# Performance work log

Measured on AMD Instinct MI355X. Metric: run time of the kernel, lower is better.

## Reference

```python
import jax, jax.numpy as jnp
import numpy as np

B, S, D_IN, D_H = 8, 4096, 256, 512
EPS = 1e-6


def setup_inputs() -> dict:
    key = jax.random.key(0)
    ks = jax.random.split(key, 5)
    scale = 1.0 / np.sqrt(D_IN)  # torch Linear default init scale (uniform bound)
    x = jax.random.normal(ks[0], (B, S, D_IN), dtype=jnp.float32)
    Wi = jax.random.normal(ks[1], (D_IN, D_H), dtype=jnp.float32) * scale
    Wf = jax.random.normal(ks[2], (D_IN, D_H), dtype=jnp.float32) * scale
    Wo = jax.random.normal(ks[3], (D_IN, D_H), dtype=jnp.float32) * scale
    Wz = jax.random.normal(ks[4], (D_IN, D_H), dtype=jnp.float32) * scale
    zb = jnp.zeros((D_H,), dtype=jnp.float32)
    return {"x": x, "Wi": Wi, "bi": zb, "Wf": Wf, "bf": zb,
            "Wo": Wo, "bo": zb, "Wz": Wz, "bz": zb}


def _xlstm_forward(x, Wi, bi, Wf, bf, Wo, bo, Wz, bz):
    # Batched projections over all timesteps at once: [B,S,D_H] each.
    i_t = jnp.exp(jnp.clip(jnp.einsum('bsd,dh->bsh', x, Wi) + bi, -20.0, 0.0))
    f_t = jnp.exp(jnp.clip(jnp.einsum('bsd,dh->bsh', x, Wf) + bf, -20.0, 0.0))
    o_t = jax.nn.sigmoid(jnp.einsum('bsd,dh->bsh', x, Wo) + bo)
    z_t = jnp.tanh(jnp.einsum('bsd,dh->bsh', x, Wz) + bz)

    def step(carry, gates):
        c, n = carry
        i, f, o, z = gates
        c = f * c + i * z
        n = f * n + i
        h = o * (c / (n + EPS))
        return (c, n), h

    c0 = jnp.zeros((x.shape[0], Wi.shape[1]), dtype=x.dtype)
    n0 = jnp.ones((x.shape[0], Wi.shape[1]), dtype=x.dtype)
    # time-major scan over the recurrence
    gates_tm = tuple(jnp.swapaxes(g, 0, 1) for g in (i_t, f_t, o_t, z_t))  # [S,B,H]
    _, h_tm = jax.lax.scan(step, (c0, n0), gates_tm)
    return jnp.swapaxes(h_tm, 0, 1)  # [B,S,H]


def reference(x, Wi, bi, Wf, bf, Wo, bo, Wz, bz):
    return _xlstm_forward(x, Wi, bi, Wf, bf, Wo, bo, Wz, bz)
```

## Files before the change

### kernel.cpp

```cpp
#include <hip/hip_runtime.h>
#include <hip/hip_bf16.h>
#include <cstdint>
#include <cstddef>

typedef __hip_bfloat16 bf16;
typedef __attribute__((ext_vector_type(8))) short short8;
typedef __attribute__((ext_vector_type(4))) short short4v;
typedef __attribute__((ext_vector_type(4))) float floatx4;

#define BB 8
#define SS 4096
#define DIN 256
#define DH 512
#define NCH 256
#define CHUNK 16

__device__ __forceinline__ float sh2f(short v) {
    unsigned int u = ((unsigned int)(unsigned short)v) << 16;
    float f; __builtin_memcpy(&f, &u, 4); return f;
}
__device__ __forceinline__ float frcp(float x) { return __builtin_amdgcn_rcpf(x); }
__device__ __forceinline__ short f2sh(float a) {
    bf16 bv = __float2bfloat16(a);
    short sv; __builtin_memcpy(&sv, &bv, 2); return sv;
}

__global__ __launch_bounds__(256) void convert_x(
    const float* __restrict__ X, bf16* __restrict__ Xb)
{
    const int idx = blockIdx.x * 256 + threadIdx.x;
    float4 v = ((const float4*)X)[idx];
    bf16 o[4] = {__float2bfloat16(v.x), __float2bfloat16(v.y),
                 __float2bfloat16(v.z), __float2bfloat16(v.w)};
    ((short4v*)Xb)[idx] = *(const short4v*)o;
}

__global__ __launch_bounds__(256) void transpose_w(
    const float* __restrict__ Wi, const float* __restrict__ Wf,
    const float* __restrict__ Wo, const float* __restrict__ Wz,
    bf16* __restrict__ Wt)
{
    int o = blockIdx.x * 256 + threadIdx.x;
    int r = o >> 8;
    int k = o & 255;
    int y = r >> 7;
    int c = r & 127;
    int g = c >> 5;
    int h = y * 32 + (c & 31);
    const float* W = (g == 0) ? Wi : (g == 1) ? Wf : (g == 2) ? Wo : Wz;
    Wt[o] = __float2bfloat16(W[(size_t)k * DH + h]);
}

__device__ __forceinline__ void load16_lds(const bf16* g, short* l)
{
    __builtin_amdgcn_global_load_lds(
        (const __attribute__((address_space(1))) unsigned int*)g,
        (__attribute__((address_space(3))) unsigned int*)l,
        16, 0, 0);
}

template<int MODE>
__global__ __launch_bounds__(256) void gemm_fused(
    const bf16* __restrict__ Xb, const bf16* __restrict__ Wt,
    const float* __restrict__ bi, const float* __restrict__ bfv,
    const float* __restrict__ bo, const float* __restrict__ bz,
    float* __restrict__ Aa, float* __restrict__ Bca, float* __restrict__ Bna,
    float* __restrict__ out, int nb)
{
    __shared__ __align__(16) short smem[128 * 132];

    const int cpx = gridDim.x >> 3;
    const int logical = ((int)blockIdx.x & 7) * cpx + ((int)blockIdx.x >> 3);
    const int y  = logical & 15;
    const int m0 = (logical >> 4) * 128;
    const int n0 = y * 128;

    const int tid  = threadIdx.x;
    const int wave = tid >> 6, lane = tid & 63;
    const int wm   = (wave >> 1) * 64, wn = (wave & 1) * 64;
    const int l15  = lane & 15;
    const int q    = lane >> 4;

    floatx4 acc[4][4];
#pragma unroll
    for (int i = 0; i < 4; i++)
#pragma unroll
        for (int j = 0; j < 4; j++) acc[i][j] = (floatx4){0.f, 0.f, 0.f, 0.f};

    const int r_ld = tid >> 2;
    const int c_ld = tid & 3;
    const bf16* agp0 = Xb + (size_t)(m0 + r_ld) * DIN + c_ld * 8;
    const bf16* agp1 = Xb + (size_t)(m0 + 64 + r_ld) * DIN + c_ld * 8;
    const bf16* bgp0 = Wt + (size_t)(n0 + r_ld) * DIN + c_ld * 8;
    const bf16* bgp1 = Wt + (size_t)(n0 + 64 + r_ld) * DIN + c_ld * 8;

#define STAGE(K0, BUF)                                            \
    do {                                                          \
        short* A_ = smem + (BUF) * 8192;                          \
        short* B_ = A_ + 4096;                                    \
        load16_lds(agp0 + (K0), &A_[tid * 8]);                    \
        load16_lds(agp1 + (K0), &A_[2048 + tid * 8]);             \
        load16_lds(bgp0 + (K0), &B_[tid * 8]);                    \
        load16_lds(bgp1 + (K0), &B_[2048 + tid * 8]);             \
    } while (0)

    STAGE(0, 0);
    asm volatile("s_waitcnt vmcnt(0)" ::: "memory");
    __builtin_amdgcn_s_barrier();

#pragma unroll
    for (int k = 0; k < 8; k++) {
        const int cur = k & 1;
        if (k < 7) STAGE((k + 1) * 32, cur ^ 1);
        const short* A = smem + cur * 8192;
        const short* B = A + 4096;
        short8 af[4], bfr[4];
#pragma unroll
        for (int ti = 0; ti < 4; ti++)
            af[ti] = *(const short8*)&A[(wm + ti * 16 + l15) * 32 + q * 8];
#pragma unroll
        for (int tj = 0; tj < 4; tj++)
            bfr[tj] = *(const short8*)&B[(wn + tj * 16 + l15) * 32 + q * 8];
#pragma unroll
        for (int ti = 0; ti < 4; ti++)
#pragma unroll
            for (int tj = 0; tj < 4; tj++)
                acc[ti][tj] = __builtin_amdgcn_mfma_f32_16x16x32_bf16(
                    af[ti], bfr[tj], acc[ti][tj], 0, 0, 0);
        asm volatile("s_waitcnt vmcnt(0) lgkmcnt(0)" ::: "memory");
        __builtin_amdgcn_s_barrier();
    }
#undef STAGE

#pragma unroll
    for (int ti = 0; ti < 4; ti++) {
        const int mrow = wm + ti * 16 + q * 4;
#pragma unroll
        for (int tj = 0; tj < 4; tj++) {
            const int cb = wn + tj * 16;
            const int g  = cb >> 5;
            if (MODE == 0 && g == 2) continue;
            const int c  = cb + l15;
            const float* bp = (g == 0) ? bi : (g == 1) ? bfv
                            : (g == 2) ? bo : bz;
            const float bsv = bp[y * 32 + (c & 31)];
#pragma unroll
            for (int r = 0; r < 4; r++) {
                const float v = acc[ti][tj][r] + bsv;
                float a;
                if (g == 0 || g == 1) {
                    a = __expf(fminf(fmaxf(v, -20.f), 0.f));
                } else if (g == 2) {
                    a = frcp(1.f + __expf(-v));
                } else {
                    a = 1.f - 2.f * frcp(__expf(2.f * v) + 1.f);
                }
                smem[(mrow + r) * 132 + c] = f2sh(a);
            }
        }
    }
    __syncthreads();

    const int bidx = m0 / SS;
    const int hh   = tid & 31;
    const int ch   = tid >> 5;
    const int ch_g = ((m0 % SS) >> 4) + ch;
    const size_t cidx = (size_t)(ch_g * nb + bidx) * DH + y * 32 + hh;
    const short* base = &smem[(ch * CHUNK) * 132];

    if (MODE == 0) {
        float A = 1.f, Bc = 0.f, Bn = 0.f;
#pragma unroll
        for (int s = 0; s < CHUNK; s++) {
            const short* rp = base + s * 132;
            const float iv = sh2f(rp[hh]);
            const float f  = sh2f(rp[32 + hh]);
            const float zv = sh2f(rp[96 + hh]);
            Bc = fmaf(f, Bc, iv * zv);
            Bn = fmaf(f, Bn, iv);
            A *= f;
        }
        Aa[cidx] = A; Bca[cidx] = Bc; Bna[cidx] = Bn;
    } else {
        float c = Aa[cidx];
        float n = Bca[cidx];
        float* orow = out + (size_t)(m0 + ch * CHUNK) * DH + y * 32 + hh;
#pragma unroll
        for (int s = 0; s < CHUNK; s++) {
            const short* rp = base + s * 132;
            const float iv = sh2f(rp[hh]);
            const float f  = sh2f(rp[32 + hh]);
            const float ov = sh2f(rp[64 + hh]);
            const float zv = sh2f(rp[96 + hh]);
            c = fmaf(f, c, iv * zv);
            n = fmaf(f, n, iv);
            orow[(size_t)s * DH] = ov * c * frcp(n + 1e-6f);
        }
    }
}

__global__ __launch_bounds__(256) void scan_chunks(
    float* __restrict__ Aa, float* __restrict__ Bca,
    const float* __restrict__ Bna, int nb)
{
    __shared__ float sA[4][64], sBc[4][64], sBn[4][64];
    const int tid = threadIdx.x;
    const int t   = blockIdx.x * 64 + (tid & 63);
    const int s   = tid >> 6;
    const int stride = nb * DH;
    const int SEG = NCH / 4;

    float A = 1.f, Bc = 0.f, Bn = 0.f;
    for (int k = 0; k < SEG; k++) {
        const size_t cidx = (size_t)(s * SEG + k) * stride + t;
        const float a  = Aa[cidx];
        const float bc = Bca[cidx];
        const float bn = Bna[cidx];
        Bc = fmaf(a, Bc, bc);
        Bn = fmaf(a, Bn, bn);
        A *= a;
    }
    sA[s][tid & 63] = A; sBc[s][tid & 63] = Bc; sBn[s][tid & 63] = Bn;
    __syncthreads();

    float c = 0.f, n = 1.f;
#pragma unroll
    for (int s2 = 0; s2 < 3; s2++) {
        if (s2 < s) {
            const float a  = sA[s2][tid & 63];
            const float nc = fmaf(a, c, sBc[s2][tid & 63]);
            n = fmaf(a, n, sBn[s2][tid & 63]);
            c = nc;
        }
    }

    for (int k = 0; k < SEG; k++) {
        const size_t cidx = (size_t)(s * SEG + k) * stride + t;
        const float a  = Aa[cidx];
        const float bc = Bca[cidx];
        const float bn = Bna[cidx];
        Aa[cidx] = c; Bca[cidx] = n;
        const float nc = fmaf(a, c, bc);
        n = fmaf(a, n, bn);
        c = nc;
    }
}

extern "C" void kernel_launch(void* const* d_in, const int* in_sizes, int n_in,
                              void* d_out, int out_size, void* d_ws, size_t ws_size,
                              hipStream_t stream)
{
    const float* x   = (const float*)d_in[0];
    const float* Wi  = (const float*)d_in[1];
    const float* bi  = (const float*)d_in[2];
    const float* Wf  = (const float*)d_in[3];
    const float* bfv = (const float*)d_in[4];
    const float* Wo  = (const float*)d_in[5];
    const float* bo  = (const float*)d_in[6];
    const float* Wz  = (const float*)d_in[7];
    const float* bz  = (const float*)d_in[8];
    float* out = (float*)d_out;

    int nb = BB;
    while (nb > 1) {
        size_t need = (1u << 20)
                    + (size_t)nb * SS * DIN * 2
                    + 3 * (size_t)NCH * nb * DH * 4;
        if (need <= ws_size) break;
        nb >>= 1;
    }

    bf16* Wt = (bf16*)d_ws;
    bf16* Xb = (bf16*)((char*)d_ws + (1u << 20));
    float* Aa  = (float*)(Xb + (size_t)nb * SS * DIN);
    float* Bca = Aa  + (size_t)NCH * nb * DH;
    float* Bna = Bca + (size_t)NCH * nb * DH;

    transpose_w<<<2048, 256, 0, stream>>>(Wi, Wf, Wo, Wz, Wt);

    for (int b0 = 0; b0 < BB; b0 += nb) {
        const float* Xsrc = x   + (size_t)b0 * SS * DIN;
        float*       Ob   = out + (size_t)b0 * SS * DH;
        convert_x<<<nb * 1024, 256, 0, stream>>>(Xsrc, Xb);
        gemm_fused<0><<<nb * 512, 256, 0, stream>>>(
            Xb, Wt, bi, bfv, bo, bz, Aa, Bca, Bna, nullptr, nb);
        scan_chunks<<<nb * 8, 256, 0, stream>>>(Aa, Bca, Bna, nb);
        gemm_fused<1><<<nb * 512, 256, 0, stream>>>(
            Xb, Wt, bi, bfv, bo, bz, Aa, Bca, Bna, Ob, nb);
    }
}
```

Measured before the change: 241.8 us.

## Fuse two-pass GEMM and chunk scan into single-pass decoupled-lookback kernel

Replaces the two-pass scheme (a GEMM with state computation, a separate scan kernel, then a second GEMM pass) with one GEMM kernel. Blocks take ordered tickets through an atomic counter and pass the carried (c, n) state to the next time tile of the same chain through flags in global memory. This removes the second GEMM over all inputs and the separate scan launch. It also merges the weight transpose, x conversion and flag reset into one prep kernel. The cost is a serial dependency chain of 32 tiles per (batch, column-group) with spin-waits between them, which may expose latency.

After: 488.9 us. +102.2%, slower.

```diff
diff --git a/kernel.cpp b/kernel.cpp
--- a/kernel.cpp
+++ b/kernel.cpp
@@ -12,7 +12,6 @@
 #define SS 4096
 #define DIN 256
 #define DH 512
-#define NCH 256
 #define CHUNK 16
 
 __device__ __forceinline__ float sh2f(short v) {
@@ -25,30 +24,36 @@
     short sv; __builtin_memcpy(&sv, &bv, 2); return sv;
 }
 
-__global__ __launch_bounds__(256) void convert_x(
-    const float* __restrict__ X, bf16* __restrict__ Xb)
-{
-    const int idx = blockIdx.x * 256 + threadIdx.x;
-    float4 v = ((const float4*)X)[idx];
-    bf16 o[4] = {__float2bfloat16(v.x), __float2bfloat16(v.y),
-                 __float2bfloat16(v.z), __float2bfloat16(v.w)};
-    ((short4v*)Xb)[idx] = *(const short4v*)o;
-}
-
-__global__ __launch_bounds__(256) void transpose_w(
+__global__ __launch_bounds__(256) void prep(
     const float* __restrict__ Wi, const float* __restrict__ Wf,
     const float* __restrict__ Wo, const float* __restrict__ Wz,
-    bf16* __restrict__ Wt)
-{
-    int o = blockIdx.x * 256 + threadIdx.x;
-    int r = o >> 8;
-    int k = o & 255;
-    int y = r >> 7;
-    int c = r & 127;
-    int g = c >> 5;
-    int h = y * 32 + (c & 31);
-    const float* W = (g == 0) ? Wi : (g == 1) ? Wf : (g == 2) ? Wo : Wz;
-    Wt[o] = __float2bfloat16(W[(size_t)k * DH + h]);
+    bf16* __restrict__ Wt,
+    const float* __restrict__ X, bf16* __restrict__ Xb,
+    unsigned int* __restrict__ Flag,
+    int tblk, int cblk, int nwords)
+{
+    const int bx = blockIdx.x;
+    const int tid = threadIdx.x;
+    if (bx < tblk) {
+        int o = bx * 256 + tid;
+        int r = o >> 8;
+        int k = o & 255;
+        int y = r >> 7;
+        int c = r & 127;
+        int g = c >> 5;
+        int h = y * 32 + (c & 31);
+        const float* W = (g == 0) ? Wi : (g == 1) ? Wf : (g == 2) ? Wo : Wz;
+        Wt[o] = __float2bfloat16(W[(size_t)k * DH + h]);
+    } else if (bx < tblk + cblk) {
+        const int idx = (bx - tblk) * 256 + tid;
+        float4 v = ((const float4*)X)[idx];
+        bf16 o[4] = {__float2bfloat16(v.x), __float2bfloat16(v.y),
+                     __float2bfloat16(v.z), __float2bfloat16(v.w)};
+        ((short4v*)Xb)[idx] = *(const short4v*)o;
+    } else {
+        const int i = (bx - tblk - cblk) * 256 + tid;
+        if (i < nwords) Flag[i] = 0u;
+    }
 }
 
 __device__ __forceinline__ void load16_lds(const bf16* g, short* l)
@@ -59,23 +64,33 @@
         16, 0, 0);
 }
 
-template<int MODE>
-__global__ __launch_bounds__(256) void gemm_fused(
+__global__ __launch_bounds__(256) void gemm_scan(
     const bf16* __restrict__ Xb, const bf16* __restrict__ Wt,
     const float* __restrict__ bi, const float* __restrict__ bfv,
     const float* __restrict__ bo, const float* __restrict__ bz,
-    float* __restrict__ Aa, float* __restrict__ Bca, float* __restrict__ Bna,
-    float* __restrict__ out, int nb)
+    float* __restrict__ Inc, unsigned int* __restrict__ Flag,
+    unsigned int* __restrict__ Tick,
+    float* __restrict__ out, int chShift)
 {
     __shared__ __align__(16) short smem[128 * 132];
-
-    const int cpx = gridDim.x >> 3;
-    const int logical = ((int)blockIdx.x & 7) * cpx + ((int)blockIdx.x >> 3);
-    const int y  = logical & 15;
-    const int m0 = (logical >> 4) * 128;
-    const int n0 = y * 128;
+    __shared__ float cA[8][32], cBc[8][32], cBn[8][32];
+    __shared__ float sc[8][32], sn[8][32];
+    __shared__ int s_ticket;
 
     const int tid  = threadIdx.x;
+    if (tid == 0)
+        s_ticket = (int)__hip_atomic_fetch_add(Tick, 1u, __ATOMIC_RELAXED,
+                                               __HIP_MEMORY_SCOPE_AGENT);
+    __syncthreads();
+    const int t     = s_ticket;
+    const int CH    = 1 << chShift;
+    const int chain = t & (CH - 1);
+    const int mt    = t >> chShift;
+    const int b     = chain >> 4;
+    const int y     = chain & 15;
+    const int m0    = (b * 32 + mt) * 128;
+    const int n0    = y * 128;
+
     const int wave = tid >> 6, lane = tid & 63;
     const int wm   = (wave >> 1) * 64, wn = (wave & 1) * 64;
     const int l15  = lane & 15;
@@ -139,7 +154,6 @@
         for (int tj = 0; tj < 4; tj++) {
             const int cb = wn + tj * 16;
             const int g  = cb >> 5;
-            if (MODE == 0 && g == 2) continue;
             const int c  = cb + l15;
             const float* bp = (g == 0) ? bi : (g == 1) ? bfv
                             : (g == 2) ? bo : bz;
@@ -161,14 +175,11 @@
     }
     __syncthreads();
 
-    const int bidx = m0 / SS;
-    const int hh   = tid & 31;
-    const int ch   = tid >> 5;
-    const int ch_g = ((m0 % SS) >> 4) + ch;
-    const size_t cidx = (size_t)(ch_g * nb + bidx) * DH + y * 32 + hh;
+    const int hh = tid & 31;
+    const int ch = tid >> 5;
     const short* base = &smem[(ch * CHUNK) * 132];
 
-    if (MODE == 0) {
+    {
         float A = 1.f, Bc = 0.f, Bn = 0.f;
 #pragma unroll
         for (int s = 0; s < CHUNK; s++) {
@@ -180,10 +191,42 @@
             Bn = fmaf(f, Bn, iv);
             A *= f;
         }
-        Aa[cidx] = A; Bca[cidx] = Bc; Bna[cidx] = Bn;
-    } else {
-        float c = Aa[cidx];
-        float n = Bca[cidx];
+        cA[ch][hh] = A; cBc[ch][hh] = Bc; cBn[ch][hh] = Bn;
+    }
+    __syncthreads();
+
+    if (tid < 32) {
+        float c = 0.f, n = 1.f;
+        if (mt > 0) {
+            const int pt = t - CH;
+            while (__hip_atomic_load(Flag + pt, __ATOMIC_ACQUIRE,
+                                     __HIP_MEMORY_SCOPE_AGENT) == 0u)
+                __builtin_amdgcn_s_sleep(2);
+            c = __hip_atomic_load(Inc + (size_t)pt * 64 + hh,
+                                  __ATOMIC_RELAXED, __HIP_MEMORY_SCOPE_AGENT);
+            n = __hip_atomic_load(Inc + (size_t)pt * 64 + 32 + hh,
+                                  __ATOMIC_RELAXED, __HIP_MEMORY_SCOPE_AGENT);
+        }
+#pragma unroll
+        for (int k = 0; k < 8; k++) {
+            sc[k][hh] = c; sn[k][hh] = n;
+            const float a  = cA[k][hh];
+            const float nc = fmaf(a, c, cBc[k][hh]);
+            n = fmaf(a, n, cBn[k][hh]);
+            c = nc;
+        }
+        __hip_atomic_store(Inc + (size_t)t * 64 + hh, c,
+                           __ATOMIC_RELAXED, __HIP_MEMORY_SCOPE_AGENT);
+        __hip_atomic_store(Inc + (size_t)t * 64 + 32 + hh, n,
+                           __ATOMIC_RELAXED, __HIP_MEMORY_SCOPE_AGENT);
+        __hip_atomic_store(Flag + t, 1u,
+                           __ATOMIC_RELEASE, __HIP_MEMORY_SCOPE_AGENT);
+    }
+    __syncthreads();
+
+    {
+        float c = sc[ch][hh];
+        float n = sn[ch][hh];
         float* orow = out + (size_t)(m0 + ch * CHUNK) * DH + y * 32 + hh;
 #pragma unroll
         for (int s = 0; s < CHUNK; s++) {
@@ -196,53 +239,6 @@
             n = fmaf(f, n, iv);
             orow[(size_t)s * DH] = ov * c * frcp(n + 1e-6f);
         }
-    }
-}
-
-__global__ __launch_bounds__(256) void scan_chunks(
-    float* __restrict__ Aa, float* __restrict__ Bca,
-    const float* __restrict__ Bna, int nb)
-{
-    __shared__ float sA[4][64], sBc[4][64], sBn[4][64];
-    const int tid = threadIdx.x;
-    const int t   = blockIdx.x * 64 + (tid & 63);
-    const int s   = tid >> 6;
-    const int stride = nb * DH;
-    const int SEG = NCH / 4;
-
-    float A = 1.f, Bc = 0.f, Bn = 0.f;
-    for (int k = 0; k < SEG; k++) {
-        const size_t cidx = (size_t)(s * SEG + k) * stride + t;
-        const float a  = Aa[cidx];
-        const float bc = Bca[cidx];
-        const float bn = Bna[cidx];
-        Bc = fmaf(a, Bc, bc);
-        Bn = fmaf(a, Bn, bn);
-        A *= a;
-    }
-    sA[s][tid & 63] = A; sBc[s][tid & 63] = Bc; sBn[s][tid & 63] = Bn;
-    __syncthreads();
-
-    float c = 0.f, n = 1.f;
-#pragma unroll
-    for (int s2 = 0; s2 < 3; s2++) {
-        if (s2 < s) {
-            const float a  = sA[s2][tid & 63];
-            const float nc = fmaf(a, c, sBc[s2][tid & 63]);
-            n = fmaf(a, n, sBn[s2][tid & 63]);
-            c = nc;
-        }
-    }
-
-    for (int k = 0; k < SEG; k++) {
-        const size_t cidx = (size_t)(s * SEG + k) * stride + t;
-        const float a  = Aa[cidx];
-        const float bc = Bca[cidx];
-        const float bn = Bna[cidx];
-        Aa[cidx] = c; Bca[cidx] = n;
-        const float nc = fmaf(a, c, bc);
-        n = fmaf(a, n, bn);
-        c = nc;
     }
 }
 
@@ -265,27 +261,31 @@
     while (nb > 1) {
         size_t need = (1u << 20)
                     + (size_t)nb * SS * DIN * 2
-                    + 3 * (size_t)NCH * nb * DH * 4;
+                    + (size_t)nb * 512 * 64 * 4
+                    + ((size_t)nb * 512 + 1) * 4;
         if (need <= ws_size) break;
         nb >>= 1;
     }
 
     bf16* Wt = (bf16*)d_ws;
     bf16* Xb = (bf16*)((char*)d_ws + (1u << 20));
-    float* Aa  = (float*)(Xb + (size_t)nb * SS * DIN);
-    float* Bca = Aa  + (size_t)NCH * nb * DH;
-    float* Bna = Bca + (size_t)NCH * nb * DH;
-
-    transpose_w<<<2048, 256, 0, stream>>>(Wi, Wf, Wo, Wz, Wt);
+    float* Inc = (float*)(Xb + (size_t)nb * SS * DIN);
+    unsigned int* Flag = (unsigned int*)(Inc + (size_t)nb * 512 * 64);
+    unsigned int* Tick = Flag + (size_t)nb * 512;
+
+    int chShift = 4;
+    { int v = nb * 16; chShift = 31 - __builtin_clz(v); }
 
     for (int b0 = 0; b0 < BB; b0 += nb) {
         const float* Xsrc = x   + (size_t)b0 * SS * DIN;
         float*       Ob   = out + (size_t)b0 * SS * DH;
-        convert_x<<<nb * 1024, 256, 0, stream>>>(Xsrc, Xb);
-        gemm_fused<0><<<nb * 512, 256, 0, stream>>>(
-            Xb, Wt, bi, bfv, bo, bz, Aa, Bca, Bna, nullptr, nb);
-        scan_chunks<<<nb * 8, 256, 0, stream>>>(Aa, Bca, Bna, nb);
-        gemm_fused<1><<<nb * 512, 256, 0, stream>>>(
-            Xb, Wt, bi, bfv, bo, bz, Aa, Bca, Bna, Ob, nb);
-    }
-}
+        const int tblk   = (b0 == 0) ? 2048 : 0;
+        const int cblk   = nb * 1024;
+        const int nwords = nb * 512 + 1;
+        const int fblk   = (nwords + 255) / 256;
+        prep<<<tblk + cblk + fblk, 256, 0, stream>>>(
+            Wi, Wf, Wo, Wz, Wt, Xsrc, Xb, Flag, tblk, cblk, nwords);
+        gemm_scan<<<nb * 512, 256, 0, stream>>>(
+            Xb, Wt, bi, bfv, bo, bz, Inc, Flag, Tick, Ob, chShift);
+    }
+}
```

## Fuse transpose, convert, two GEMM passes and scan into one cooperative kernel

Applied to the files above, without the earlier changes.

Replaces the five separate launches (weight transpose, x conversion, GEMM pass 0, chunk scan, GEMM pass 1) with a single persistent cooperative kernel that separates the phases with grid-wide syncs. GEMM tiles are walked in a grid-stride loop sized to occupancy. The aim is to remove launch gaps and tail effects between the stages. In exchange it adds grid-sync cost, fixes the grid size by occupancy, and runs the scan phase on only a few blocks while the rest sit idle.

After: 512.5 us. +111.9%, slower.

```diff
diff --git a/kernel.cpp b/kernel.cpp
--- a/kernel.cpp
+++ b/kernel.cpp
@@ -1,7 +1,10 @@
 #include <hip/hip_runtime.h>
+#include <hip/hip_cooperative_groups.h>
 #include <hip/hip_bf16.h>
 #include <cstdint>
 #include <cstddef>
+
+namespace cg = cooperative_groups;
 
 typedef __hip_bfloat16 bf16;
 typedef __attribute__((ext_vector_type(8))) short short8;
@@ -25,32 +28,6 @@
     short sv; __builtin_memcpy(&sv, &bv, 2); return sv;
 }
 
-__global__ __launch_bounds__(256) void convert_x(
-    const float* __restrict__ X, bf16* __restrict__ Xb)
-{
-    const int idx = blockIdx.x * 256 + threadIdx.x;
-    float4 v = ((const float4*)X)[idx];
-    bf16 o[4] = {__float2bfloat16(v.x), __float2bfloat16(v.y),
-                 __float2bfloat16(v.z), __float2bfloat16(v.w)};
-    ((short4v*)Xb)[idx] = *(const short4v*)o;
-}
-
-__global__ __launch_bounds__(256) void transpose_w(
-    const float* __restrict__ Wi, const float* __restrict__ Wf,
-    const float* __restrict__ Wo, const float* __restrict__ Wz,
-    bf16* __restrict__ Wt)
-{
-    int o = blockIdx.x * 256 + threadIdx.x;
-    int r = o >> 8;
-    int k = o & 255;
-    int y = r >> 7;
-    int c = r & 127;
-    int g = c >> 5;
-    int h = y * 32 + (c & 31);
-    const float* W = (g == 0) ? Wi : (g == 1) ? Wf : (g == 2) ? Wo : Wz;
-    Wt[o] = __float2bfloat16(W[(size_t)k * DH + h]);
-}
-
 __device__ __forceinline__ void load16_lds(const bf16* g, short* l)
 {
     __builtin_amdgcn_global_load_lds(
@@ -60,19 +37,17 @@
 }
 
 template<int MODE>
-__global__ __launch_bounds__(256) void gemm_fused(
+__device__ __forceinline__ void gemm_tile(
+    short* __restrict__ smem, int logical, int nb,
     const bf16* __restrict__ Xb, const bf16* __restrict__ Wt,
     const float* __restrict__ bi, const float* __restrict__ bfv,
     const float* __restrict__ bo, const float* __restrict__ bz,
     float* __restrict__ Aa, float* __restrict__ Bca, float* __restrict__ Bna,
-    float* __restrict__ out, int nb)
+    float* __restrict__ out)
 {
-    __shared__ __align__(16) short smem[128 * 132];
-
-    const int cpx = gridDim.x >> 3;
-    const int logical = ((int)blockIdx.x & 7) * cpx + ((int)blockIdx.x >> 3);
     const int y  = logical & 15;
-    const int m0 = (logical >> 4) * 128;
+    const int gm = logical >> 4;
+    const int m0 = gm * 128;
     const int n0 = y * 128;
 
     const int tid  = threadIdx.x;
@@ -93,6 +68,8 @@
     const bf16* agp1 = Xb + (size_t)(m0 + 64 + r_ld) * DIN + c_ld * 8;
     const bf16* bgp0 = Wt + (size_t)(n0 + r_ld) * DIN + c_ld * 8;
     const bf16* bgp1 = Wt + (size_t)(n0 + 64 + r_ld) * DIN + c_ld * 8;
+
+    __syncthreads();
 
 #define STAGE(K0, BUF)                                            \
     do {                                                          \
@@ -199,50 +176,107 @@
     }
 }
 
-__global__ __launch_bounds__(256) void scan_chunks(
-    float* __restrict__ Aa, float* __restrict__ Bca,
-    const float* __restrict__ Bna, int nb)
+extern "C" __global__ void __launch_bounds__(256) fused_all(
+    const float* __restrict__ Wi, const float* __restrict__ Wf,
+    const float* __restrict__ Wo, const float* __restrict__ Wz,
+    const float* __restrict__ X,
+    bf16* __restrict__ Wt, bf16* __restrict__ Xb,
+    const float* __restrict__ bi, const float* __restrict__ bfv,
+    const float* __restrict__ bo, const float* __restrict__ bz,
+    float* __restrict__ Aa, float* __restrict__ Bca, float* __restrict__ Bna,
+    float* __restrict__ out, int nb, int doTrans)
 {
-    __shared__ float sA[4][64], sBc[4][64], sBn[4][64];
+    __shared__ __align__(16) short smem[128 * 132];
+    cg::grid_group grid = cg::this_grid();
+
     const int tid = threadIdx.x;
-    const int t   = blockIdx.x * 64 + (tid & 63);
-    const int s   = tid >> 6;
-    const int stride = nb * DH;
-    const int SEG = NCH / 4;
-
-    float A = 1.f, Bc = 0.f, Bn = 0.f;
-    for (int k = 0; k < SEG; k++) {
-        const size_t cidx = (size_t)(s * SEG + k) * stride + t;
-        const float a  = Aa[cidx];
-        const float bc = Bca[cidx];
-        const float bn = Bna[cidx];
-        Bc = fmaf(a, Bc, bc);
-        Bn = fmaf(a, Bn, bn);
-        A *= a;
-    }
-    sA[s][tid & 63] = A; sBc[s][tid & 63] = Bc; sBn[s][tid & 63] = Bn;
-    __syncthreads();
-
-    float c = 0.f, n = 1.f;
-#pragma unroll
-    for (int s2 = 0; s2 < 3; s2++) {
-        if (s2 < s) {
-            const float a  = sA[s2][tid & 63];
-            const float nc = fmaf(a, c, sBc[s2][tid & 63]);
-            n = fmaf(a, n, sBn[s2][tid & 63]);
+    const int bid = blockIdx.x;
+    const int G   = gridDim.x;
+    const int gt  = bid * 256 + tid;
+    const int NTH = G * 256;
+
+    if (doTrans) {
+        for (int o = gt; o < 2048 * 256; o += NTH) {
+            int r = o >> 8, k = o & 255;
+            int y = r >> 7, c = r & 127;
+            int g = c >> 5, h = y * 32 + (c & 31);
+            const float* W = (g == 0) ? Wi : (g == 1) ? Wf : (g == 2) ? Wo : Wz;
+            Wt[o] = __float2bfloat16(W[(size_t)k * DH + h]);
+        }
+    }
+    {
+        const int nvec = nb * SS * DIN / 4;
+        for (int i = gt; i < nvec; i += NTH) {
+            float4 v = ((const float4*)X)[i];
+            bf16 o4[4] = {__float2bfloat16(v.x), __float2bfloat16(v.y),
+                          __float2bfloat16(v.z), __float2bfloat16(v.w)};
+            ((short4v*)Xb)[i] = *(const short4v*)o4;
+        }
+    }
+    __threadfence();
+    grid.sync();
+
+    const int NT  = nb * 512;
+    const int cpx = NT >> 3;
+    for (int d = bid; d < NT; d += G) {
+        const int logical = ((d & 7) * cpx) + (d >> 3);
+        gemm_tile<0>(smem, logical, nb, Xb, Wt, bi, bfv, bo, bz,
+                     Aa, Bca, Bna, out);
+    }
+    __threadfence();
+    grid.sync();
+
+    if (bid < nb * 8) {
+        float* sA  = (float*)smem;
+        float* sBc = sA + 256;
+        float* sBn = sBc + 256;
+        const int l  = tid & 63;
+        const int t  = bid * 64 + l;
+        const int s  = tid >> 6;
+        const int stride = nb * DH;
+        const int SEG = NCH / 4;
+
+        float A = 1.f, Bc = 0.f, Bn = 0.f;
+        for (int k = 0; k < SEG; k++) {
+            const size_t cidx = (size_t)(s * SEG + k) * stride + t;
+            const float a  = Aa[cidx];
+            const float bc = Bca[cidx];
+            const float bn = Bna[cidx];
+            Bc = fmaf(a, Bc, bc);
+            Bn = fmaf(a, Bn, bn);
+            A *= a;
+        }
+        sA[s * 64 + l] = A; sBc[s * 64 + l] = Bc; sBn[s * 64 + l] = Bn;
+        __syncthreads();
+
+        float c = 0.f, n = 1.f;
+#pragma unroll
+        for (int s2 = 0; s2 < 3; s2++) {
+            if (s2 < s) {
+                const float a  = sA[s2 * 64 + l];
+                const float nc = fmaf(a, c, sBc[s2 * 64 + l]);
+                n = fmaf(a, n, sBn[s2 * 64 + l]);
+                c = nc;
+            }
+        }
+        for (int k = 0; k < SEG; k++) {
+            const size_t cidx = (size_t)(s * SEG + k) * stride + t;
+            const float a  = Aa[cidx];
+            const float bc = Bca[cidx];
+            const float bn = Bna[cidx];
+            Aa[cidx] = c; Bca[cidx] = n;
+            const float nc = fmaf(a, c, bc);
+            n = fmaf(a, n, bn);
             c = nc;
         }
     }
-
-    for (int k = 0; k < SEG; k++) {
-        const size_t cidx = (size_t)(s * SEG + k) * stride + t;
-        const float a  = Aa[cidx];
-        const float bc = Bca[cidx];
-        const float bn = Bna[cidx];
-        Aa[cidx] = c; Bca[cidx] = n;
-        const float nc = fmaf(a, c, bc);
-        n = fmaf(a, n, bn);
-        c = nc;
+    __threadfence();
+    grid.sync();
+
+    for (int d = bid; d < NT; d += G) {
+        const int logical = ((d & 7) * cpx) + (d >> 3);
+        gemm_tile<1>(smem, logical, nb, Xb, Wt, bi, bfv, bo, bz,
+                     Aa, Bca, Bna, out);
     }
 }
 
@@ -276,16 +310,30 @@
     float* Bca = Aa  + (size_t)NCH * nb * DH;
     float* Bna = Bca + (size_t)NCH * nb * DH;
 
-    transpose_w<<<2048, 256, 0, stream>>>(Wi, Wf, Wo, Wz, Wt);
+    static int maxB = -1;
+    if (maxB < 0) {
+        if (hipOccupancyMaxActiveBlocksPerMultiprocessor(
+                &maxB, (const void*)fused_all, 256, 0) != hipSuccess || maxB < 1)
+            maxB = 1;
+        if (maxB > 8) maxB = 8;
+    }
+    const int NUM_CU = 256;
 
     for (int b0 = 0; b0 < BB; b0 += nb) {
         const float* Xsrc = x   + (size_t)b0 * SS * DIN;
         float*       Ob   = out + (size_t)b0 * SS * DH;
-        convert_x<<<nb * 1024, 256, 0, stream>>>(Xsrc, Xb);
-        gemm_fused<0><<<nb * 512, 256, 0, stream>>>(
-            Xb, Wt, bi, bfv, bo, bz, Aa, Bca, Bna, nullptr, nb);
-        scan_chunks<<<nb * 8, 256, 0, stream>>>(Aa, Bca, Bna, nb);
-        gemm_fused<1><<<nb * 512, 256, 0, stream>>>(
-            Xb, Wt, bi, bfv, bo, bz, Aa, Bca, Bna, Ob, nb);
-    }
-}
+        int G = maxB * NUM_CU;
+        if (G > nb * 512) G = nb * 512;
+        int nbArg = nb;
+        int doT = (b0 == 0) ? 1 : 0;
+        void* args[] = {
+            (void*)&Wi, (void*)&Wf, (void*)&Wo, (void*)&Wz,
+            (void*)&Xsrc, (void*)&Wt, (void*)&Xb,
+            (void*)&bi, (void*)&bfv, (void*)&bo, (void*)&bz,
+            (void*)&Aa, (void*)&Bca, (void*)&Bna,
+            (void*)&Ob, (void*)&nbArg, (void*)&doT
+        };
+        hipLaunchCooperativeKernel((const void*)fused_all,
+                                   dim3(G), dim3(256), args, 0, stream);
+    }
+}
```
